# Kernel optimization log

Measured on AMD Instinct MI355X. Metric: run time of the kernel, lower is better.

Reference implementation:

```python
import jax, jax.numpy as jnp
import numpy as np

BSZ, D = 256, 512
LOGIT_SCALE = 1.0


def setup_inputs() -> dict:
    key = jax.random.key(0)
    k1, k2, k3 = jax.random.split(key, 3)
    x = jax.random.normal(k1, (BSZ, D), dtype=jnp.float32)
    y = jax.random.normal(k2, (BSZ, D), dtype=jnp.float32)
    z = jax.random.normal(k3, (BSZ, D), dtype=jnp.float32)
    return {"x": x, "y": y, "z": z}


def _logits_n_squared(anchor, a, b, shift):
    # torch recursion: products[i*bsz + r] = a[r] * roll(b, i)[r] = a[r] * b[(r - i) % bsz]
    bsz = anchor.shape[0]
    P = a[None, :, :] * b[shift]              # (i, r, d) = (bsz, bsz, d)
    logits = jnp.einsum('ad,ird->air', anchor, P)  # (a, i, r)
    return LOGIT_SCALE * logits.reshape(bsz, bsz * bsz)


def _cross_entropy_diag(logits):
    bsz = logits.shape[0]
    lp = jax.nn.log_softmax(logits, axis=-1)
    idx = jnp.arange(bsz)
    return -jnp.mean(lp[idx, idx])


def reference(x, y, z):
    bsz = x.shape[0]
    r = jnp.arange(bsz)
    shift = (r[None, :] - r[:, None]) % bsz   # (i, r): index into b after roll by i
    reps = [x, y, z]
    losses = []
    for i in range(3):
        anchor = reps[i]
        non_anchor = [reps[j] for j in range(3) if j != i]
        logits = _logits_n_squared(anchor, non_anchor[0], non_anchor[1], shift)
        losses.append(_cross_entropy_diag(logits))
    return sum(losses) / 3.0
```

## Files before the change

### kernel.cpp

```cpp
#include <hip/hip_runtime.h>

#define DIM 512

typedef unsigned int uint;
typedef unsigned short ushort;
typedef __attribute__((ext_vector_type(8))) short short8;
typedef __attribute__((ext_vector_type(4))) float f32x4;

__device__ __forceinline__ uint pack_bf16(float a, float b) {
    union { float f; uint u; } ua, ub;
    ua.f = a; ub.f = b;
    uint x0 = ua.u + 0x8000u;
    uint x1 = ub.u + 0x8000u;
    return __builtin_amdgcn_perm(x1, x0, 0x07060302);
}

__device__ __forceinline__ uint mul_pack(uint u, float xl, float xh) {
    union { float f; uint u; } lo, hi, a, b;
    lo.u = u << 16;
    hi.u = u & 0xffff0000u;
    a.f = lo.f * xl;
    b.f = hi.f * xh;
    return __builtin_amdgcn_perm(b.u + 0x8000u, a.u + 0x8000u, 0x07060302);
}

__global__ void conv_swizzle(const float* __restrict__ z, const float* __restrict__ y,
                             ushort* __restrict__ zbf, ushort* __restrict__ ybf) {
    int t = blockIdx.x * 256 + threadIdx.x;
    int idx = t & 16383;
    const float* src = (t < 16384) ? z : y;
    ushort* dst = (t < 16384) ? zbf : ybf;
    int r15  = idx & 15;
    int quad = (idx >> 4) & 3;
    int kt   = (idx >> 6) & 15;
    int g    = idx >> 10;
    const float* p = src + (g * 16 + r15) * DIM + kt * 32 + quad * 8;
    float4 a = *(const float4*)(p);
    float4 b = *(const float4*)(p + 4);
    uint4 o;
    o.x = pack_bf16(a.x, a.y);
    o.y = pack_bf16(a.z, a.w);
    o.z = pack_bf16(b.x, b.y);
    o.w = pack_bf16(b.z, b.w);
    *(uint4*)(dst + idx * 8) = o;
}

__global__ void __launch_bounds__(512, 2)
gemm_fused(const float* __restrict__ x, const float* __restrict__ y,
           const float* __restrict__ z,
           const ushort* __restrict__ ybf, const ushort* __restrict__ zbf,
           float* __restrict__ rowM, float* __restrict__ rowS,
           float* __restrict__ colM, float* __restrict__ colS,
           float* __restrict__ diag, uint* __restrict__ counter) {
    __shared__ __align__(16) float xs[DIM];
    __shared__ float redA[128 * 4];
    __shared__ float rowMaxS[128];
    __shared__ float redB[256 * 2];
    __shared__ float colMaxS[256];
    __shared__ float dred[8];

    const int tid = threadIdx.x;
    const int a   = blockIdx.x >> 1;
    const int rt  = blockIdx.x & 1;

    if (blockIdx.x == 0 && tid == 0) *counter = 0u;

    const int lane = tid & 63;
    const int wave = tid >> 6;
    const int quad = lane >> 4;
    const int ln15 = lane & 15;
    const int wr = wave >> 2;
    const int wc = wave & 3;

    float xv = x[a * DIM + tid];
    xs[tid] = xv;

    if (rt == 0) {
        float p = xv * y[a * DIM + tid] * z[a * DIM + tid];
        #pragma unroll
        for (int m = 1; m < 64; m <<= 1) p += __shfl_xor(p, m, 64);
        if (lane == 0) dred[wave] = p;
    }
    __syncthreads();
    if (rt == 0 && tid == 0) {
        float s = 0.f;
        #pragma unroll
        for (int w2 = 0; w2 < 8; ++w2) s += dred[w2];
        diag[a] = s;
    }

    f32x4 acc[4][4];
    #pragma unroll
    for (int i = 0; i < 4; ++i)
        #pragma unroll
        for (int j = 0; j < 4; ++j)
            acc[i][j] = (f32x4){0.f, 0.f, 0.f, 0.f};

    const ushort* ybase = ybf + (rt * 8 + wr * 4) * 8192 + lane * 8;
    const ushort* zbase = zbf + (wc * 4) * 8192 + lane * 8;

    uint4 zu[2][4], yu[2][4];
    #pragma unroll
    for (int j = 0; j < 4; ++j)
        zu[0][j] = *(const uint4*)(zbase + j * 8192);
    #pragma unroll
    for (int i = 0; i < 4; ++i)
        yu[0][i] = *(const uint4*)(ybase + i * 8192);

    #pragma unroll 2
    for (int kt = 0; kt < 16; ++kt) {
        const int cur = kt & 1, nxt = cur ^ 1;
        if (kt < 15) {
            #pragma unroll
            for (int j = 0; j < 4; ++j)
                zu[nxt][j] = *(const uint4*)(zbase + j * 8192 + (kt + 1) * 512);
            #pragma unroll
            for (int i = 0; i < 4; ++i)
                yu[nxt][i] = *(const uint4*)(ybase + i * 8192 + (kt + 1) * 512);
        }
        float4 x0 = *(const float4*)(xs + kt * 32 + quad * 8);
        float4 x1 = *(const float4*)(xs + kt * 32 + quad * 8 + 4);

        short8 af[4], bfr[4];
        #pragma unroll
        for (int j = 0; j < 4; ++j)
            bfr[j] = *(short8*)&zu[cur][j];
        #pragma unroll
        for (int i = 0; i < 4; ++i) {
            uint4 o;
            o.x = mul_pack(yu[cur][i].x, x0.x, x0.y);
            o.y = mul_pack(yu[cur][i].y, x0.z, x0.w);
            o.z = mul_pack(yu[cur][i].z, x1.x, x1.y);
            o.w = mul_pack(yu[cur][i].w, x1.z, x1.w);
            af[i] = *(short8*)&o;
        }
        #pragma unroll
        for (int i = 0; i < 4; ++i)
            #pragma unroll
            for (int j = 0; j < 4; ++j)
                acc[i][j] = __builtin_amdgcn_mfma_f32_16x16x32_bf16(af[i], bfr[j], acc[i][j], 0, 0, 0);
    }
    __syncthreads();

    #pragma unroll
    for (int i = 0; i < 4; ++i) {
        #pragma unroll
        for (int reg = 0; reg < 4; ++reg) {
            float m = fmaxf(fmaxf(acc[i][0][reg], acc[i][1][reg]),
                            fmaxf(acc[i][2][reg], acc[i][3][reg]));
            #pragma unroll
            for (int d = 1; d < 16; d <<= 1) m = fmaxf(m, __shfl_xor(m, d, 64));
            if (ln15 == 0) redA[(wr * 64 + i * 16 + quad * 4 + reg) * 4 + wc] = m;
        }
    }
    __syncthreads();
    if (tid < 128) {
        float m = fmaxf(fmaxf(redA[tid * 4 + 0], redA[tid * 4 + 1]),
                        fmaxf(redA[tid * 4 + 2], redA[tid * 4 + 3]));
        rowMaxS[tid] = m;
    }
    __syncthreads();
    #pragma unroll
    for (int i = 0; i < 4; ++i) {
        #pragma unroll
        for (int reg = 0; reg < 4; ++reg) {
            int r = wr * 64 + i * 16 + quad * 4 + reg;
            float rm = rowMaxS[r];
            float s = __expf(acc[i][0][reg] - rm) + __expf(acc[i][1][reg] - rm)
                    + __expf(acc[i][2][reg] - rm) + __expf(acc[i][3][reg] - rm);
            #pragma unroll
            for (int d = 1; d < 16; d <<= 1) s += __shfl_xor(s, d, 64);
            if (ln15 == 0) redA[r * 4 + wc] = s;
        }
    }
    __syncthreads();
    if (tid < 128) {
        float s = redA[tid * 4 + 0] + redA[tid * 4 + 1] + redA[tid * 4 + 2] + redA[tid * 4 + 3];
        int rg = rt * 128 + tid;
        rowM[a * 256 + rg] = rowMaxS[tid];
        rowS[a * 256 + rg] = s;
    }

    #pragma unroll
    for (int j = 0; j < 4; ++j) {
        float m = -3.4e38f;
        #pragma unroll
        for (int i = 0; i < 4; ++i)
            #pragma unroll
            for (int reg = 0; reg < 4; ++reg)
                m = fmaxf(m, acc[i][j][reg]);
        m = fmaxf(m, __shfl_xor(m, 16, 64));
        m = fmaxf(m, __shfl_xor(m, 32, 64));
        if (quad == 0) redB[(wc * 64 + j * 16 + ln15) * 2 + wr] = m;
    }
    __syncthreads();
    if (tid < 256) colMaxS[tid] = fmaxf(redB[tid * 2], redB[tid * 2 + 1]);
    __syncthreads();
    #pragma unroll
    for (int j = 0; j < 4; ++j) {
        int n = wc * 64 + j * 16 + ln15;
        float cm = colMaxS[n];
        float s = 0.f;
        #pragma unroll
        for (int i = 0; i < 4; ++i)
            #pragma unroll
            for (int reg = 0; reg < 4; ++reg)
                s += __expf(acc[i][j][reg] - cm);
        s += __shfl_xor(s, 16, 64);
        s += __shfl_xor(s, 32, 64);
        if (quad == 0) redB[n * 2 + wr] = s;
    }
    __syncthreads();
    if (tid < 256) {
        float s = redB[tid * 2] + redB[tid * 2 + 1];
        colM[(a * 256 + tid) * 2 + rt] = colMaxS[tid];
        colS[(a * 256 + tid) * 2 + rt] = s;
    }
}

__device__ __forceinline__ float blk_max(float v, float* sm) {
    #pragma unroll
    for (int d = 1; d < 64; d <<= 1) v = fmaxf(v, __shfl_xor(v, d, 64));
    __syncthreads();
    if ((threadIdx.x & 63) == 0) sm[threadIdx.x >> 6] = v;
    __syncthreads();
    return fmaxf(fmaxf(sm[0], sm[1]), fmaxf(sm[2], sm[3]));
}
__device__ __forceinline__ float blk_sum(float v, float* sm) {
    #pragma unroll
    for (int d = 1; d < 64; d <<= 1) v += __shfl_xor(v, d, 64);
    __syncthreads();
    if ((threadIdx.x & 63) == 0) sm[threadIdx.x >> 6] = v;
    __syncthreads();
    return sm[0] + sm[1] + sm[2] + sm[3];
}

__global__ void combine_final(const float* __restrict__ rowM, const float* __restrict__ rowS,
                              const float* __restrict__ colM, const float* __restrict__ colS,
                              const float* __restrict__ diag,
                              float* __restrict__ m123, uint* __restrict__ counter,
                              float* __restrict__ out) {
    __shared__ float sm[4];
    __shared__ uint isLast;
    int b = blockIdx.x, t = threadIdx.x;
    float m = rowM[b * 256 + t], s = rowS[b * 256 + t];
    float M = blk_max(m, sm);
    float S = blk_sum(s * __expf(m - M), sm);
    float M1 = M + __logf(S);
    m = rowM[t * 256 + b]; s = rowS[t * 256 + b];
    M = blk_max(m, sm);
    S = blk_sum(s * __expf(m - M), sm);
    float M2 = M + __logf(S);
    float am = colM[(t * 256 + b) * 2 + 0], av = colS[(t * 256 + b) * 2 + 0];
    float bm = colM[(t * 256 + b) * 2 + 1], bv = colS[(t * 256 + b) * 2 + 1];
    m = fmaxf(am, bm);
    s = av * __expf(am - m) + bv * __expf(bm - m);
    M = blk_max(m, sm);
    S = blk_sum(s * __expf(m - M), sm);
    float M3 = M + __logf(S);
    if (t == 0) {
        m123[b] = M1 + M2 + M3;
        __threadfence();
        isLast = (atomicAdd(counter, 1u) == 255u) ? 1u : 0u;
    }
    __syncthreads();
    if (isLast) {
        __threadfence();
        const volatile float* vm = (const volatile float*)m123;
        const volatile float* vd = (const volatile float*)diag;
        float S1 = blk_sum(vm[t], sm);
        float S2 = blk_sum(vd[t], sm);
        if (t == 0) out[0] = S1 / 768.0f - S2 / 256.0f;
    }
}

extern "C" void kernel_launch(void* const* d_in, const int* in_sizes, int n_in,
                              void* d_out, int out_size, void* d_ws, size_t ws_size,
                              hipStream_t stream) {
    const float* x = (const float*)d_in[0];
    const float* y = (const float*)d_in[1];
    const float* z = (const float*)d_in[2];
    char* w = (char*)d_ws;
    ushort* zbf = (ushort*)(w);
    ushort* ybf = (ushort*)(w + 262144);
    float* rowM = (float*)(w + 524288);
    float* rowS = (float*)(w + 786432);
    float* colM = (float*)(w + 1048576);
    float* colS = (float*)(w + 1572864);
    float* diag = (float*)(w + 2097152);
    float* m123 = (float*)(w + 2098176);
    uint*  counter = (uint*)(w + 2099200);
    float* out  = (float*)d_out;

    conv_swizzle<<<128, 256, 0, stream>>>(z, y, zbf, ybf);
    gemm_fused<<<512, 512, 0, stream>>>(x, y, z, ybf, zbf, rowM, rowS, colM, colS, diag, counter);
    combine_final<<<256, 256, 0, stream>>>(rowM, rowS, colM, colS, diag, m123, counter, out);
}
```

Before: 113.0 us.

## Split fused GEMM into single-wave tiles and defer partial softmax merging

```diff
diff --git a/kernel.cpp b/kernel.cpp
--- a/kernel.cpp
+++ b/kernel.cpp
@@ -45,88 +45,56 @@
     *(uint4*)(dst + idx * 8) = o;
 }
 
-__global__ void __launch_bounds__(512, 2)
-gemm_fused(const float* __restrict__ x, const float* __restrict__ y,
-           const float* __restrict__ z,
-           const ushort* __restrict__ ybf, const ushort* __restrict__ zbf,
-           float* __restrict__ rowM, float* __restrict__ rowS,
-           float* __restrict__ colM, float* __restrict__ colS,
-           float* __restrict__ diag, uint* __restrict__ counter) {
-    __shared__ __align__(16) float xs[DIM];
-    __shared__ float redA[128 * 4];
-    __shared__ float rowMaxS[128];
-    __shared__ float redB[256 * 2];
-    __shared__ float colMaxS[256];
-    __shared__ float dred[8];
-
-    const int tid = threadIdx.x;
-    const int a   = blockIdx.x >> 1;
-    const int rt  = blockIdx.x & 1;
-
-    if (blockIdx.x == 0 && tid == 0) *counter = 0u;
-
-    const int lane = tid & 63;
-    const int wave = tid >> 6;
+__global__ void __launch_bounds__(64, 4)
+gemm_tile(const float* __restrict__ x,
+          const ushort* __restrict__ ybf, const ushort* __restrict__ zbf,
+          float* __restrict__ rowMp, float* __restrict__ rowSp,
+          float* __restrict__ colMp, float* __restrict__ colSp,
+          uint* __restrict__ counter) {
+    const int bid = blockIdx.x;
+    if (bid == 0 && threadIdx.x == 0) *counter = 0u;
+
+    const int a  = bid >> 5;
+    const int rt = (bid >> 2) & 7;
+    const int ct = bid & 3;
+    const int lane = threadIdx.x;
     const int quad = lane >> 4;
     const int ln15 = lane & 15;
-    const int wr = wave >> 2;
-    const int wc = wave & 3;
-
-    float xv = x[a * DIM + tid];
-    xs[tid] = xv;
-
-    if (rt == 0) {
-        float p = xv * y[a * DIM + tid] * z[a * DIM + tid];
-        #pragma unroll
-        for (int m = 1; m < 64; m <<= 1) p += __shfl_xor(p, m, 64);
-        if (lane == 0) dred[wave] = p;
-    }
-    __syncthreads();
-    if (rt == 0 && tid == 0) {
-        float s = 0.f;
-        #pragma unroll
-        for (int w2 = 0; w2 < 8; ++w2) s += dred[w2];
-        diag[a] = s;
-    }
-
-    f32x4 acc[4][4];
-    #pragma unroll
-    for (int i = 0; i < 4; ++i)
+
+    const ushort* ybase = ybf + (rt * 2) * 8192 + lane * 8;
+    const ushort* zbase = zbf + (ct * 4) * 8192 + lane * 8;
+    const float*  xrow  = x + a * DIM + quad * 8;
+
+    f32x4 acc[2][4];
+    #pragma unroll
+    for (int i = 0; i < 2; ++i)
         #pragma unroll
         for (int j = 0; j < 4; ++j)
             acc[i][j] = (f32x4){0.f, 0.f, 0.f, 0.f};
 
-    const ushort* ybase = ybf + (rt * 8 + wr * 4) * 8192 + lane * 8;
-    const ushort* zbase = zbf + (wc * 4) * 8192 + lane * 8;
-
-    uint4 zu[2][4], yu[2][4];
-    #pragma unroll
-    for (int j = 0; j < 4; ++j)
-        zu[0][j] = *(const uint4*)(zbase + j * 8192);
-    #pragma unroll
-    for (int i = 0; i < 4; ++i)
-        yu[0][i] = *(const uint4*)(ybase + i * 8192);
+    uint4 yu[2][2], zu[2][4];
+    #pragma unroll
+    for (int i = 0; i < 2; ++i) yu[0][i] = *(const uint4*)(ybase + i * 8192);
+    #pragma unroll
+    for (int j = 0; j < 4; ++j) zu[0][j] = *(const uint4*)(zbase + j * 8192);
 
     #pragma unroll 2
     for (int kt = 0; kt < 16; ++kt) {
         const int cur = kt & 1, nxt = cur ^ 1;
         if (kt < 15) {
             #pragma unroll
+            for (int i = 0; i < 2; ++i)
+                yu[nxt][i] = *(const uint4*)(ybase + i * 8192 + (kt + 1) * 512);
+            #pragma unroll
             for (int j = 0; j < 4; ++j)
                 zu[nxt][j] = *(const uint4*)(zbase + j * 8192 + (kt + 1) * 512);
-            #pragma unroll
-            for (int i = 0; i < 4; ++i)
-                yu[nxt][i] = *(const uint4*)(ybase + i * 8192 + (kt + 1) * 512);
-        }
-        float4 x0 = *(const float4*)(xs + kt * 32 + quad * 8);
-        float4 x1 = *(const float4*)(xs + kt * 32 + quad * 8 + 4);
-
-        short8 af[4], bfr[4];
-        #pragma unroll
-        for (int j = 0; j < 4; ++j)
-            bfr[j] = *(short8*)&zu[cur][j];
-        #pragma unroll
-        for (int i = 0; i < 4; ++i) {
+        }
+        float4 x0 = *(const float4*)(xrow + kt * 32);
+        float4 x1 = *(const float4*)(xrow + kt * 32 + 4);
+
+        short8 af[2], bfr[4];
+        #pragma unroll
+        for (int i = 0; i < 2; ++i) {
             uint4 o;
             o.x = mul_pack(yu[cur][i].x, x0.x, x0.y);
             o.y = mul_pack(yu[cur][i].y, x0.z, x0.w);
@@ -135,86 +103,57 @@
             af[i] = *(short8*)&o;
         }
         #pragma unroll
-        for (int i = 0; i < 4; ++i)
+        for (int j = 0; j < 4; ++j)
+            bfr[j] = *(short8*)&zu[cur][j];
+        #pragma unroll
+        for (int i = 0; i < 2; ++i)
             #pragma unroll
             for (int j = 0; j < 4; ++j)
                 acc[i][j] = __builtin_amdgcn_mfma_f32_16x16x32_bf16(af[i], bfr[j], acc[i][j], 0, 0, 0);
     }
-    __syncthreads();
-
-    #pragma unroll
-    for (int i = 0; i < 4; ++i) {
+
+    #pragma unroll
+    for (int i = 0; i < 2; ++i) {
         #pragma unroll
         for (int reg = 0; reg < 4; ++reg) {
             float m = fmaxf(fmaxf(acc[i][0][reg], acc[i][1][reg]),
                             fmaxf(acc[i][2][reg], acc[i][3][reg]));
             #pragma unroll
             for (int d = 1; d < 16; d <<= 1) m = fmaxf(m, __shfl_xor(m, d, 64));
-            if (ln15 == 0) redA[(wr * 64 + i * 16 + quad * 4 + reg) * 4 + wc] = m;
-        }
-    }
-    __syncthreads();
-    if (tid < 128) {
-        float m = fmaxf(fmaxf(redA[tid * 4 + 0], redA[tid * 4 + 1]),
-                        fmaxf(redA[tid * 4 + 2], redA[tid * 4 + 3]));
-        rowMaxS[tid] = m;
-    }
-    __syncthreads();
-    #pragma unroll
-    for (int i = 0; i < 4; ++i) {
-        #pragma unroll
-        for (int reg = 0; reg < 4; ++reg) {
-            int r = wr * 64 + i * 16 + quad * 4 + reg;
-            float rm = rowMaxS[r];
-            float s = __expf(acc[i][0][reg] - rm) + __expf(acc[i][1][reg] - rm)
-                    + __expf(acc[i][2][reg] - rm) + __expf(acc[i][3][reg] - rm);
+            float s = __expf(acc[i][0][reg] - m) + __expf(acc[i][1][reg] - m)
+                    + __expf(acc[i][2][reg] - m) + __expf(acc[i][3][reg] - m);
             #pragma unroll
             for (int d = 1; d < 16; d <<= 1) s += __shfl_xor(s, d, 64);
-            if (ln15 == 0) redA[r * 4 + wc] = s;
-        }
-    }
-    __syncthreads();
-    if (tid < 128) {
-        float s = redA[tid * 4 + 0] + redA[tid * 4 + 1] + redA[tid * 4 + 2] + redA[tid * 4 + 3];
-        int rg = rt * 128 + tid;
-        rowM[a * 256 + rg] = rowMaxS[tid];
-        rowS[a * 256 + rg] = s;
-    }
-
+            if (ln15 == 0) {
+                int r = rt * 32 + i * 16 + quad * 4 + reg;
+                rowMp[(a * 4 + ct) * 256 + r] = m;
+                rowSp[(a * 4 + ct) * 256 + r] = s;
+            }
+        }
+    }
     #pragma unroll
     for (int j = 0; j < 4; ++j) {
         float m = -3.4e38f;
         #pragma unroll
-        for (int i = 0; i < 4; ++i)
+        for (int i = 0; i < 2; ++i)
             #pragma unroll
             for (int reg = 0; reg < 4; ++reg)
                 m = fmaxf(m, acc[i][j][reg]);
         m = fmaxf(m, __shfl_xor(m, 16, 64));
         m = fmaxf(m, __shfl_xor(m, 32, 64));
-        if (quad == 0) redB[(wc * 64 + j * 16 + ln15) * 2 + wr] = m;
-    }
-    __syncthreads();
-    if (tid < 256) colMaxS[tid] = fmaxf(redB[tid * 2], redB[tid * 2 + 1]);
-    __syncthreads();
-    #pragma unroll
-    for (int j = 0; j < 4; ++j) {
-        int n = wc * 64 + j * 16 + ln15;
-        float cm = colMaxS[n];
         float s = 0.f;
         #pragma unroll
-        for (int i = 0; i < 4; ++i)
+        for (int i = 0; i < 2; ++i)
             #pragma unroll
             for (int reg = 0; reg < 4; ++reg)
-                s += __expf(acc[i][j][reg] - cm);
+                s += __expf(acc[i][j][reg] - m);
         s += __shfl_xor(s, 16, 64);
         s += __shfl_xor(s, 32, 64);
-        if (quad == 0) redB[n * 2 + wr] = s;
-    }
-    __syncthreads();
-    if (tid < 256) {
-        float s = redB[tid * 2] + redB[tid * 2 + 1];
-        colM[(a * 256 + tid) * 2 + rt] = colMaxS[tid];
-        colS[(a * 256 + tid) * 2 + rt] = s;
+        if (quad == 0) {
+            int sg = ct * 64 + j * 16 + ln15;
+            colMp[(a * 8 + rt) * 256 + sg] = m;
+            colSp[(a * 8 + rt) * 256 + sg] = s;
+        }
     }
 }
 
@@ -235,31 +174,61 @@
     return sm[0] + sm[1] + sm[2] + sm[3];
 }
 
-__global__ void combine_final(const float* __restrict__ rowM, const float* __restrict__ rowS,
-                              const float* __restrict__ colM, const float* __restrict__ colS,
-                              const float* __restrict__ diag,
+__global__ void combine_final(const float* __restrict__ rowMp, const float* __restrict__ rowSp,
+                              const float* __restrict__ colMp, const float* __restrict__ colSp,
+                              const float* __restrict__ x, const float* __restrict__ y,
+                              const float* __restrict__ z,
                               float* __restrict__ m123, uint* __restrict__ counter,
                               float* __restrict__ out) {
     __shared__ float sm[4];
     __shared__ uint isLast;
     int b = blockIdx.x, t = threadIdx.x;
-    float m = rowM[b * 256 + t], s = rowS[b * 256 + t];
-    float M = blk_max(m, sm);
-    float S = blk_sum(s * __expf(m - M), sm);
+
+    float lm = -3.4e38f, ls = 0.f;
+    #pragma unroll
+    for (int c = 0; c < 4; ++c) {
+        float m = rowMp[(b * 4 + c) * 256 + t];
+        float s = rowSp[(b * 4 + c) * 256 + t];
+        float nm = fmaxf(lm, m);
+        ls = ls * __expf(lm - nm) + s * __expf(m - nm);
+        lm = nm;
+    }
+    float M = blk_max(lm, sm);
+    float S = blk_sum(ls * __expf(lm - M), sm);
     float M1 = M + __logf(S);
-    m = rowM[t * 256 + b]; s = rowS[t * 256 + b];
-    M = blk_max(m, sm);
-    S = blk_sum(s * __expf(m - M), sm);
+
+    lm = -3.4e38f; ls = 0.f;
+    #pragma unroll
+    for (int c = 0; c < 4; ++c) {
+        float m = rowMp[(t * 4 + c) * 256 + b];
+        float s = rowSp[(t * 4 + c) * 256 + b];
+        float nm = fmaxf(lm, m);
+        ls = ls * __expf(lm - nm) + s * __expf(m - nm);
+        lm = nm;
+    }
+    M = blk_max(lm, sm);
+    S = blk_sum(ls * __expf(lm - M), sm);
     float M2 = M + __logf(S);
-    float am = colM[(t * 256 + b) * 2 + 0], av = colS[(t * 256 + b) * 2 + 0];
-    float bm = colM[(t * 256 + b) * 2 + 1], bv = colS[(t * 256 + b) * 2 + 1];
-    m = fmaxf(am, bm);
-    s = av * __expf(am - m) + bv * __expf(bm - m);
-    M = blk_max(m, sm);
-    S = blk_sum(s * __expf(m - M), sm);
+
+    lm = -3.4e38f; ls = 0.f;
+    #pragma unroll
+    for (int r = 0; r < 8; ++r) {
+        float m = colMp[(t * 8 + r) * 256 + b];
+        float s = colSp[(t * 8 + r) * 256 + b];
+        float nm = fmaxf(lm, m);
+        ls = ls * __expf(lm - nm) + s * __expf(m - nm);
+        lm = nm;
+    }
+    M = blk_max(lm, sm);
+    S = blk_sum(ls * __expf(lm - M), sm);
     float M3 = M + __logf(S);
+
+    float d = x[b * DIM + t] * y[b * DIM + t] * z[b * DIM + t]
+            + x[b * DIM + 256 + t] * y[b * DIM + 256 + t] * z[b * DIM + 256 + t];
+    float D = blk_sum(d, sm);
+
     if (t == 0) {
-        m123[b] = M1 + M2 + M3;
+        m123[b] = M1 + M2 + M3 - 3.0f * D;
         __threadfence();
         isLast = (atomicAdd(counter, 1u) == 255u) ? 1u : 0u;
     }
@@ -267,10 +236,8 @@
     if (isLast) {
         __threadfence();
         const volatile float* vm = (const volatile float*)m123;
-        const volatile float* vd = (const volatile float*)diag;
         float S1 = blk_sum(vm[t], sm);
-        float S2 = blk_sum(vd[t], sm);
-        if (t == 0) out[0] = S1 / 768.0f - S2 / 256.0f;
+        if (t == 0) out[0] = S1 / 768.0f;
     }
 }
 
@@ -281,18 +248,17 @@
     const float* y = (const float*)d_in[1];
     const float* z = (const float*)d_in[2];
     char* w = (char*)d_ws;
-    ushort* zbf = (ushort*)(w);
-    ushort* ybf = (ushort*)(w + 262144);
-    float* rowM = (float*)(w + 524288);
-    float* rowS = (float*)(w + 786432);
-    float* colM = (float*)(w + 1048576);
-    float* colS = (float*)(w + 1572864);
-    float* diag = (float*)(w + 2097152);
-    float* m123 = (float*)(w + 2098176);
-    uint*  counter = (uint*)(w + 2099200);
+    ushort* zbf  = (ushort*)(w);
+    ushort* ybf  = (ushort*)(w + 262144);
+    float* rowMp = (float*)(w + 524288);
+    float* rowSp = (float*)(w + 1572864);
+    float* colMp = (float*)(w + 2621440);
+    float* colSp = (float*)(w + 4718592);
+    float* m123  = (float*)(w + 6815744);
+    uint*  counter = (uint*)(w + 6816768);
     float* out  = (float*)d_out;
 
     conv_swizzle<<<128, 256, 0, stream>>>(z, y, zbf, ybf);
-    gemm_fused<<<512, 512, 0, stream>>>(x, y, z, ybf, zbf, rowM, rowS, colM, colS, diag, counter);
-    combine_final<<<256, 256, 0, stream>>>(rowM, rowS, colM, colS, diag, m123, counter, out);
-}
+    gemm_tile<<<8192, 64, 0, stream>>>(x, ybf, zbf, rowMp, rowSp, colMp, colSp, counter);
+    combine_final<<<256, 256, 0, stream>>>(rowMp, rowSp, colMp, colSp, x, y, z, m123, counter, out);
+}
```

New measurement: 120.8 us. 6.8% more time.
